# Optimization experiments

Hardware: AMD Instinct MI355X
Metric: run time of the kernel (lower is better)

Reference implementation:

```python
import jax, jax.numpy as jnp
import numpy as np

B, TS, TT = 32, 128, 64
V_SRC, V_TRG, E, H = 30000, 30000, 256, 512


def _cell(x, h, c, Wih, Whh, b):
    # x:[B,in], h,c:[B,H]; PyTorch gate order i,f,g,o
    g = x @ Wih.T + h @ Whh.T + b
    i, f, gg, o = jnp.split(g, 4, axis=-1)
    c = jax.nn.sigmoid(f) * c + jax.nn.sigmoid(i) * jnp.tanh(gg)
    h = jax.nn.sigmoid(o) * jnp.tanh(c)
    return h, c


def _lstm2(xs, p0, p1, state):
    # xs: [T,B,in]; 2-layer LSTM (dropout disabled / eval mode)
    def step(carry, x):
        h0, c0, h1, c1 = carry
        h0, c0 = _cell(x, h0, c0, *p0)
        h1, c1 = _cell(h0, h1, c1, *p1)
        return (h0, c0, h1, c1), h1
    carry, ys = jax.lax.scan(step, state, xs)
    return ys, carry


def setup_inputs() -> dict:
    key = jax.random.key(0)
    ks = jax.random.split(key, 28)
    n = lambda k, s: jax.random.normal(k, s, dtype=jnp.float32) * 0.05
    inp = {
        'src': jax.random.randint(ks[0], (B, TS), 0, V_SRC),
        'trg': jax.random.randint(ks[1], (B, TT), 0, V_TRG),
        'enc_emb': n(ks[2], (V_SRC, E)),
        'dec_emb': n(ks[3], (V_TRG, E)),
        'enc_Wih0': n(ks[4], (4 * H, E)), 'enc_Whh0': n(ks[5], (4 * H, H)),
        'enc_b0': n(ks[6], (4 * H,)),
        'enc_Wih1': n(ks[7], (4 * H, H)), 'enc_Whh1': n(ks[8], (4 * H, H)),
        'enc_b1': n(ks[9], (4 * H,)),
        'dec_Wih0': n(ks[10], (4 * H, E)), 'dec_Whh0': n(ks[11], (4 * H, H)),
        'dec_b0': n(ks[12], (4 * H,)),
        'dec_Wih1': n(ks[13], (4 * H, H)), 'dec_Whh1': n(ks[14], (4 * H, H)),
        'dec_b1': n(ks[15], (4 * H,)),
        'fc_W': n(ks[16], (V_TRG, H)), 'fc_b': n(ks[17], (V_TRG,)),
    }
    return inp


def reference(src, trg, enc_emb, dec_emb,
              enc_Wih0, enc_Whh0, enc_b0, enc_Wih1, enc_Whh1, enc_b1,
              dec_Wih0, dec_Whh0, dec_b0, dec_Wih1, dec_Whh1, dec_b1,
              fc_W, fc_b):
    zero = jnp.zeros((B, H), dtype=jnp.float32)
    # ---- Encoder ----
    src_e = enc_emb[src]                       # [B,TS,E]
    _, enc_state = _lstm2(jnp.swapaxes(src_e, 0, 1),
                          (enc_Wih0, enc_Whh0, enc_b0),
                          (enc_Wih1, enc_Whh1, enc_b1),
                          (zero, zero, zero, zero))
    # ---- Decoder (teacher forcing = 1.0): inputs trg[:, :-1] ----
    dec_in = dec_emb[trg[:, :-1]]              # [B,TT-1,E]
    hs, _ = _lstm2(jnp.swapaxes(dec_in, 0, 1),
                   (dec_Wih0, dec_Whh0, dec_b0),
                   (dec_Wih1, dec_Whh1, dec_b1),
                   enc_state)                  # hs: [TT-1,B,H]
    logits = jnp.einsum('tbh,vh->btv', hs, fc_W) + fc_b  # [B,TT-1,V]
    # outputs[:,0,:] stays zero as in original
    out = jnp.concatenate([jnp.zeros((B, 1, V_TRG), dtype=jnp.float32), logits], axis=1)
    return out
```

## Files before the change

### kernel.cpp

```cpp
#include <hip/hip_runtime.h>
#include <hip/hip_bf16.h>

#define B_SZ 32
#define TS 128
#define TT 64
#define TD 63
#define E_DIM 256
#define H_DIM 512
#define G4 2048
#define V_TRG 30000
#define NWG_L 32

typedef __attribute__((ext_vector_type(8))) short s8v;
typedef __attribute__((ext_vector_type(4))) float f32x4;
typedef unsigned short u16;
typedef unsigned long long u64;

static __device__ __forceinline__ float sigf(float x) {
  x = fminf(fmaxf(x, -30.f), 30.f);
  return 1.0f / (1.0f + __expf(-x));
}
static __device__ __forceinline__ float tanh_(float x) {
  x = fminf(fmaxf(x, -15.f), 15.f);
  float e = __expf(2.0f * x);
  return (e - 1.0f) / (e + 1.0f);
}
static __device__ __forceinline__ u16 f2bf(float x) {
  union { float f; unsigned u; } v; v.f = x;
  unsigned r = v.u + 0x7FFF + ((v.u >> 16) & 1);
  return (u16)(r >> 16);
}

struct Cvt { const float* s; u16* d; int n; };
struct Cvt9 { Cvt m[9]; };

__global__ void cvt_kernel(Cvt9 c) {
  const Cvt cv = c.m[blockIdx.y];
  int i = blockIdx.x * 256 + threadIdx.x;
  const int stride = gridDim.x * 256;
  for (; i < cv.n; i += stride) cv.d[i] = f2bf(cv.s[i]);
}

__global__ void embed_kernel(const int* __restrict__ tok, const float* __restrict__ emb,
                             u16* __restrict__ x, int rows, int tstride) {
  int i = blockIdx.x * 256 + threadIdx.x;
  if (i >= rows * E_DIM) return;
  int e = i & (E_DIM - 1);
  int r = i >> 8;
  int b = r & 31, t = r >> 5;
  int token = tok[b * tstride + t];
  x[i] = f2bf(emb[token * E_DIM + e]);
}

template<int MODE>
__global__ __launch_bounds__(256) void gemm_bf16(
    const u16* __restrict__ A, const u16* __restrict__ Bw,
    const float* __restrict__ bias, float* __restrict__ out,
    int M, int N, int K) {
  __shared__ u16 As[128 * 40];
  __shared__ u16 Bs[128 * 40];
  const int nb = blockIdx.x, mb = blockIdx.y;
  const int tid = threadIdx.x;
  const int w = tid >> 6, lane = tid & 63, quad = lane >> 4, cc = lane & 15;
  const int wm = w & 1, wn = w >> 1;
  f32x4 acc[4][4] = {};

  for (int k0 = 0; k0 < K; k0 += 32) {
    #pragma unroll
    for (int i = tid; i < 512; i += 256) {
      int m = i >> 2, kk = (i & 3) << 3;
      int gm = mb * 128 + m;
      s8v va = {};
      if (gm < M) va = *(const s8v*)(A + (size_t)gm * K + k0 + kk);
      *(s8v*)(&As[m * 40 + kk]) = va;
      int gn = nb * 128 + m;
      s8v vb = {};
      if (gn < N) vb = *(const s8v*)(Bw + (size_t)gn * K + k0 + kk);
      *(s8v*)(&Bs[m * 40 + kk]) = vb;
    }
    __syncthreads();
    s8v af[4], bf[4];
    #pragma unroll
    for (int mt = 0; mt < 4; ++mt)
      af[mt] = *(const s8v*)(&As[(wm * 64 + mt * 16 + cc) * 40 + quad * 8]);
    #pragma unroll
    for (int nt = 0; nt < 4; ++nt)
      bf[nt] = *(const s8v*)(&Bs[(wn * 64 + nt * 16 + cc) * 40 + quad * 8]);
    #pragma unroll
    for (int mt = 0; mt < 4; ++mt)
      #pragma unroll
      for (int nt = 0; nt < 4; ++nt)
        acc[mt][nt] = __builtin_amdgcn_mfma_f32_16x16x32_bf16(af[mt], bf[nt], acc[mt][nt], 0, 0, 0);
    __syncthreads();
  }

  #pragma unroll
  for (int mt = 0; mt < 4; ++mt)
    #pragma unroll
    for (int nt = 0; nt < 4; ++nt) {
      int col = nb * 128 + wn * 64 + nt * 16 + cc;
      if (col >= N) continue;
      float bv = bias[col];
      #pragma unroll
      for (int r = 0; r < 4; ++r) {
        int row = mb * 128 + wm * 64 + mt * 16 + quad * 4 + r;
        if (row >= M) continue;
        float v = acc[mt][nt][r] + bv;
        if (MODE == 0) {
          out[(size_t)row * N + col] = v;
        } else {
          int t = row >> 5, b = row & 31;
          out[(size_t)b * (TT * V_TRG) + (size_t)(t + 1) * V_TRG + col] = v;
        }
      }
    }
}

static __device__ __forceinline__ void spin_until(int* p, int target) {
  while (__hip_atomic_load(p, __ATOMIC_RELAXED, __HIP_MEMORY_SCOPE_AGENT) < target)
    __builtin_amdgcn_s_sleep(1);
}

__global__ __launch_bounds__(128, 1) void lstm2_scan(
    const float* __restrict__ Gx,
    const u16* __restrict__ Whh0,
    const u16* __restrict__ Wih1,
    const u16* __restrict__ Whh1,
    const float* __restrict__ b1,
    const u16* __restrict__ h0i, const float* __restrict__ c0i,
    const u16* __restrict__ h1i, const float* __restrict__ c1i,
    u16* __restrict__ H0x,
    u16* __restrict__ H1x,
    u16* __restrict__ h0f, float* __restrict__ c0f,
    u16* __restrict__ h1f, float* __restrict__ c1f,
    int T, int* bar0, int* bar1) {
  __shared__ u16 BsH[64 * 512];
  __shared__ u16 BsX[64 * 512];
  const bool L1 = (blockIdx.x >= NWG_L);
  const int jn = blockIdx.x & 31;
  const int tid = threadIdx.x;
  const int mt = tid >> 6, lane = tid & 63, quad = lane >> 4, cc = lane & 15;

  {
    const u16* Wh = L1 ? Whh1 : Whh0;
    for (int i = tid; i < 64 * 64; i += 128) {
      int col = i >> 6, kc = i & 63;
      int g = col >> 4, c = col & 15;
      int row = g * 512 + jn * 16 + c;
      s8v v = *(const s8v*)(Wh + (size_t)row * 512 + kc * 8);
      int kcs = (kc + col) & 63;
      *(s8v*)(&BsH[col * 512 + kcs * 8]) = v;
    }
    if (L1) {
      for (int i = tid; i < 64 * 64; i += 128) {
        int col = i >> 6, kc = i & 63;
        int g = col >> 4, c = col & 15;
        int row = g * 512 + jn * 16 + c;
        s8v v = *(const s8v*)(Wih1 + (size_t)row * 512 + kc * 8);
        int kcs = (kc + col) & 63;
        *(s8v*)(&BsX[col * 512 + kcs * 8]) = v;
      }
    }
  }
  __syncthreads();

  const int b0 = mt * 16 + quad * 4;
  const int j = jn * 16 + cc;
  const int arow = (mt * 16 + cc) * H_DIM + quad * 8;

  f32x4 creg;
  {
    const float* ci = L1 ? c1i : c0i;
    #pragma unroll
    for (int r = 0; r < 4; ++r) creg[r] = ci[(b0 + r) * H_DIM + j];
  }

  if (!L1) {
    for (int s = 0; s < T; ++s) {
      float gx[4][4];
      #pragma unroll
      for (int g = 0; g < 4; ++g)
        #pragma unroll
        for (int r = 0; r < 4; ++r)
          gx[g][r] = Gx[(size_t)(s * B_SZ + b0 + r) * G4 + g * 512 + j];

      if (s > 0) {
        spin_until(bar0, NWG_L * s);
        asm volatile("" ::: "memory");
      }
      const u16* hsrc = (s == 0) ? h0i : (H0x + (size_t)(s - 1) * (B_SZ * H_DIM));
      f32x4 acc[4] = {};
      #pragma unroll
      for (int ks = 0; ks < 16; ++ks) {
        s8v a = *(const s8v*)(hsrc + arow + ks * 32);
        int kc = ks * 4 + quad;
        #pragma unroll
        for (int g = 0; g < 4; ++g) {
          int col = g * 16 + cc;
          int kcs = (kc + col) & 63;
          s8v bw = *(const s8v*)(&BsH[col * 512 + kcs * 8]);
          acc[g] = __builtin_amdgcn_mfma_f32_16x16x32_bf16(a, bw, acc[g], 0, 0, 0);
        }
      }
      u16* hw = H0x + (size_t)s * (B_SZ * H_DIM);
      #pragma unroll
      for (int r = 0; r < 4; ++r) {
        float gi = acc[0][r] + gx[0][r];
        float gf = acc[1][r] + gx[1][r];
        float gg = acc[2][r] + gx[2][r];
        float go = acc[3][r] + gx[3][r];
        float cn = sigf(gf) * creg[r] + sigf(gi) * tanh_(gg);
        float hn = sigf(go) * tanh_(cn);
        creg[r] = cn;
        u16 hb = f2bf(hn);
        __hip_atomic_store(&hw[(b0 + r) * H_DIM + j], hb,
                           __ATOMIC_RELAXED, __HIP_MEMORY_SCOPE_AGENT);
        if (s == T - 1) {
          h0f[(b0 + r) * H_DIM + j] = hb;
          c0f[(b0 + r) * H_DIM + j] = cn;
        }
      }
      __syncthreads();
      if (tid == 0)
        __hip_atomic_fetch_add(bar0, 1, __ATOMIC_RELAXED, __HIP_MEMORY_SCOPE_AGENT);
    }
  } else {
    float bv4[4];
    #pragma unroll
    for (int g = 0; g < 4; ++g) bv4[g] = b1[g * 512 + j];

    for (int s = 0; s < T; ++s) {
      spin_until(bar0, NWG_L * (s + 1));
      asm volatile("" ::: "memory");
      const u16* h0src = H0x + (size_t)s * (B_SZ * H_DIM);
      s8v a0r[16];
      #pragma unroll
      for (int ks = 0; ks < 16; ++ks)
        a0r[ks] = *(const s8v*)(h0src + arow + ks * 32);

      if (s > 0) {
        spin_until(bar1, NWG_L * s);
        asm volatile("" ::: "memory");
      }
      const u16* h1src = (s == 0) ? h1i : (H1x + (size_t)(s - 1) * (B_SZ * H_DIM));
      f32x4 acc[4] = {};
      #pragma unroll
      for (int ks = 0; ks < 16; ++ks) {
        s8v a1 = *(const s8v*)(h1src + arow + ks * 32);
        int kc = ks * 4 + quad;
        #pragma unroll
        for (int g = 0; g < 4; ++g) {
          int col = g * 16 + cc;
          int kcs = (kc + col) & 63;
          s8v bh = *(const s8v*)(&BsH[col * 512 + kcs * 8]);
          s8v bx = *(const s8v*)(&BsX[col * 512 + kcs * 8]);
          acc[g] = __builtin_amdgcn_mfma_f32_16x16x32_bf16(a1, bh, acc[g], 0, 0, 0);
          acc[g] = __builtin_amdgcn_mfma_f32_16x16x32_bf16(a0r[ks], bx, acc[g], 0, 0, 0);
        }
      }
      u16* hw = H1x + (size_t)s * (B_SZ * H_DIM);
      #pragma unroll
      for (int r = 0; r < 4; ++r) {
        float gi = acc[0][r] + bv4[0];
        float gf = acc[1][r] + bv4[1];
        float gg = acc[2][r] + bv4[2];
        float go = acc[3][r] + bv4[3];
        float cn = sigf(gf) * creg[r] + sigf(gi) * tanh_(gg);
        float hn = sigf(go) * tanh_(cn);
        creg[r] = cn;
        u16 hb = f2bf(hn);
        __hip_atomic_store(&hw[(b0 + r) * H_DIM + j], hb,
                           __ATOMIC_RELAXED, __HIP_MEMORY_SCOPE_AGENT);
        if (s == T - 1) {
          h1f[(b0 + r) * H_DIM + j] = hb;
          c1f[(b0 + r) * H_DIM + j] = cn;
        }
      }
      __syncthreads();
      if (tid == 0 && s < T - 1)
        __hip_atomic_fetch_add(bar1, 1, __ATOMIC_RELAXED, __HIP_MEMORY_SCOPE_AGENT);
    }
  }
}

__global__ void zero_t0_kernel(float* __restrict__ out) {
  int i = blockIdx.x * 256 + threadIdx.x;
  if (i >= B_SZ * V_TRG) return;
  int b = i / V_TRG, v = i - b * V_TRG;
  out[(size_t)b * (TT * V_TRG) + v] = 0.f;
}

extern "C" void kernel_launch(void* const* d_in, const int* in_sizes, int n_in,
                              void* d_out, int out_size, void* d_ws, size_t ws_size,
                              hipStream_t stream) {
  const int*   src     = (const int*)d_in[0];
  const int*   trg     = (const int*)d_in[1];
  const float* enc_emb = (const float*)d_in[2];
  const float* dec_emb = (const float*)d_in[3];
  const float* eW0i = (const float*)d_in[4];
  const float* eW0h = (const float*)d_in[5];
  const float* eb0  = (const float*)d_in[6];
  const float* eW1i = (const float*)d_in[7];
  const float* eW1h = (const float*)d_in[8];
  const float* eb1  = (const float*)d_in[9];
  const float* dW0i = (const float*)d_in[10];
  const float* dW0h = (const float*)d_in[11];
  const float* db0  = (const float*)d_in[12];
  const float* dW1i = (const float*)d_in[13];
  const float* dW1h = (const float*)d_in[14];
  const float* db1  = (const float*)d_in[15];
  const float* fcW  = (const float*)d_in[16];
  const float* fcb  = (const float*)d_in[17];
  float* out = (float*)d_out;

  char* ws = (char*)d_ws;
  size_t off = 0;
  auto alloc = [&](size_t bytes) {
    char* p = ws + off;
    off = (off + bytes + 255) & ~(size_t)255;
    return p;
  };
  int*   bar    = (int*)alloc(1024);
  u16*   hzero  = (u16*)alloc(B_SZ * H_DIM * 2);
  float* czero  = (float*)alloc(B_SZ * H_DIM * 4);
  u16* eW0i_b = (u16*)alloc((size_t)G4 * E_DIM * 2);
  u16* eW0h_b = (u16*)alloc((size_t)G4 * H_DIM * 2);
  u16* eW1i_b = (u16*)alloc((size_t)G4 * H_DIM * 2);
  u16* eW1h_b = (u16*)alloc((size_t)G4 * H_DIM * 2);
  u16* dW0i_b = (u16*)alloc((size_t)G4 * E_DIM * 2);
  u16* dW0h_b = (u16*)alloc((size_t)G4 * H_DIM * 2);
  u16* dW1i_b = (u16*)alloc((size_t)G4 * H_DIM * 2);
  u16* dW1h_b = (u16*)alloc((size_t)G4 * H_DIM * 2);
  u16* fcW_b  = (u16*)alloc((size_t)V_TRG * H_DIM * 2);
  u16* x_enc  = (u16*)alloc((size_t)TS * B_SZ * E_DIM * 2);
  u16* x_dec  = (u16*)alloc((size_t)TD * B_SZ * E_DIM * 2);
  float* Gx   = (float*)alloc((size_t)TS * B_SZ * G4 * 4);
  u16* H0e    = (u16*)alloc((size_t)TS * B_SZ * H_DIM * 2);
  u16* H1e    = (u16*)alloc((size_t)TS * B_SZ * H_DIM * 2);
  u16* H0d    = (u16*)alloc((size_t)TD * B_SZ * H_DIM * 2);
  u16* H1d    = (u16*)alloc((size_t)TD * B_SZ * H_DIM * 2);
  u16* hF0    = (u16*)alloc(B_SZ * H_DIM * 2);
  float* cF0  = (float*)alloc(B_SZ * H_DIM * 4);
  u16* hF1    = (u16*)alloc(B_SZ * H_DIM * 2);
  float* cF1  = (float*)alloc(B_SZ * H_DIM * 4);
  u16* hFd0   = (u16*)alloc(B_SZ * H_DIM * 2);
  float* cFd0 = (float*)alloc(B_SZ * H_DIM * 4);
  u16* hFd1   = (u16*)alloc(B_SZ * H_DIM * 2);
  float* cFd1 = (float*)alloc(B_SZ * H_DIM * 4);

  hipMemsetAsync(bar, 0, 1024, stream);
  hipMemsetAsync(hzero, 0, B_SZ * H_DIM * 2, stream);
  hipMemsetAsync(czero, 0, B_SZ * H_DIM * 4, stream);

  Cvt9 c9 = {{ {eW0i, eW0i_b, G4 * E_DIM}, {eW0h, eW0h_b, G4 * H_DIM},
               {eW1i, eW1i_b, G4 * H_DIM}, {eW1h, eW1h_b, G4 * H_DIM},
               {dW0i, dW0i_b, G4 * E_DIM}, {dW0h, dW0h_b, G4 * H_DIM},
               {dW1i, dW1i_b, G4 * H_DIM}, {dW1h, dW1h_b, G4 * H_DIM},
               {fcW,  fcW_b,  V_TRG * H_DIM} }};
  cvt_kernel<<<dim3(1024, 9), 256, 0, stream>>>(c9);

  embed_kernel<<<(TS * B_SZ * E_DIM + 255) / 256, 256, 0, stream>>>(src, enc_emb, x_enc, TS * B_SZ, TS);
  embed_kernel<<<(TD * B_SZ * E_DIM + 255) / 256, 256, 0, stream>>>(trg, dec_emb, x_dec, TD * B_SZ, TT);

  gemm_bf16<0><<<dim3(16, 32), 256, 0, stream>>>(x_enc, eW0i_b, eb0, Gx, TS * B_SZ, G4, E_DIM);
  lstm2_scan<<<2 * NWG_L, 128, 0, stream>>>(
      Gx, eW0h_b, eW1i_b, eW1h_b, eb1,
      hzero, czero, hzero, czero,
      H0e, H1e, hF0, cF0, hF1, cF1, TS, bar + 0, bar + 32);

  gemm_bf16<0><<<dim3(16, 16), 256, 0, stream>>>(x_dec, dW0i_b, db0, Gx, TD * B_SZ, G4, E_DIM);
  lstm2_scan<<<2 * NWG_L, 128, 0, stream>>>(
      Gx, dW0h_b, dW1i_b, dW1h_b, db1,
      hF0, cF0, hF1, cF1,
      H0d, H1d, hFd0, cFd0, hFd1, cFd1, TD, bar + 64, bar + 96);

  gemm_bf16<1><<<dim3((V_TRG + 127) / 128, (TD * B_SZ + 127) / 128), 256, 0, stream>>>(
      H1d, fcW_b, fcb, out, TD * B_SZ, V_TRG, H_DIM);
  zero_t0_kernel<<<(B_SZ * V_TRG + 255) / 256, 256, 0, stream>>>(out);
}
```

Measured before the change: 1.808 ms.

## Replace counter barriers with per-element tagged hidden states and fuse input projection

Hidden states are now stored as 32-bit words that pack the bf16 value with a timestep tag. Consumers poll the data directly until every tag matches, which removes the atomic counter barriers and the __syncthreads before each signal. The layer-0 input projection (the x·Wih0 GEMM) now runs inside the scan kernel using Wih0 held in shared memory, so the separate Gx GEMM launches and the large Gx buffer go away. In exchange, the state buffers double in size and need a memset, per-step polling loads become wider, and the decoder writes an extra plain bf16 copy of h1 for the output projection.

```diff
diff --git a/kernel.cpp b/kernel.cpp
--- a/kernel.cpp
+++ b/kernel.cpp
@@ -14,6 +14,7 @@
 typedef __attribute__((ext_vector_type(8))) short s8v;
 typedef __attribute__((ext_vector_type(4))) float f32x4;
 typedef unsigned short u16;
+typedef unsigned int u32;
 typedef unsigned long long u64;
 
 static __device__ __forceinline__ float sigf(float x) {
@@ -116,24 +117,44 @@
     }
 }
 
-static __device__ __forceinline__ void spin_until(int* p, int target) {
-  while (__hip_atomic_load(p, __ATOMIC_RELAXED, __HIP_MEMORY_SCOPE_AGENT) < target)
-    __builtin_amdgcn_s_sleep(1);
+union PK { u32 w[4]; s8v v; };
+
+static __device__ __forceinline__ void poll16(const u32* __restrict__ base, u32 tag, PK* a) {
+  const u64 tp  = (u64)tag | ((u64)tag << 32);
+  const u64 MSK = 0x0000FFFF0000FFFFULL;
+  for (;;) {
+    u64 bad = 0;
+    #pragma unroll
+    for (int ks = 0; ks < 16; ++ks) {
+      const u64* p = (const u64*)(base + ks * 32);
+      #pragma unroll
+      for (int i = 0; i < 4; ++i) {
+        u64 q = __hip_atomic_load(p + i, __ATOMIC_RELAXED, __HIP_MEMORY_SCOPE_AGENT);
+        bad |= (q ^ tp) & MSK;
+        a[ks].w[i] = (u32)(((q >> 16) & 0xFFFFULL) | ((q >> 32) & 0xFFFF0000ULL));
+      }
+    }
+    if (!__any(bad != 0)) return;
+    __builtin_amdgcn_s_sleep(2);
+  }
 }
 
 __global__ __launch_bounds__(128, 1) void lstm2_scan(
-    const float* __restrict__ Gx,
+    const u16* __restrict__ X,
+    const u16* __restrict__ Wih0,
     const u16* __restrict__ Whh0,
+    const float* __restrict__ bias0,
     const u16* __restrict__ Wih1,
     const u16* __restrict__ Whh1,
-    const float* __restrict__ b1,
+    const float* __restrict__ bias1,
     const u16* __restrict__ h0i, const float* __restrict__ c0i,
     const u16* __restrict__ h1i, const float* __restrict__ c1i,
-    u16* __restrict__ H0x,
-    u16* __restrict__ H1x,
+    u32* __restrict__ H0x,
+    u32* __restrict__ H1x,
+    u16* __restrict__ Hplain,
     u16* __restrict__ h0f, float* __restrict__ c0f,
     u16* __restrict__ h1f, float* __restrict__ c1f,
-    int T, int* bar0, int* bar1) {
+    int T) {
   __shared__ u16 BsH[64 * 512];
   __shared__ u16 BsX[64 * 512];
   const bool L1 = (blockIdx.x >= NWG_L);
@@ -145,120 +166,80 @@
     const u16* Wh = L1 ? Whh1 : Whh0;
     for (int i = tid; i < 64 * 64; i += 128) {
       int col = i >> 6, kc = i & 63;
-      int g = col >> 4, c = col & 15;
-      int row = g * 512 + jn * 16 + c;
+      int row = (col >> 4) * 512 + jn * 16 + (col & 15);
       s8v v = *(const s8v*)(Wh + (size_t)row * 512 + kc * 8);
-      int kcs = (kc + col) & 63;
-      *(s8v*)(&BsH[col * 512 + kcs * 8]) = v;
+      *(s8v*)(&BsH[col * 512 + ((kc + col) & 63) * 8]) = v;
     }
     if (L1) {
       for (int i = tid; i < 64 * 64; i += 128) {
         int col = i >> 6, kc = i & 63;
-        int g = col >> 4, c = col & 15;
-        int row = g * 512 + jn * 16 + c;
+        int row = (col >> 4) * 512 + jn * 16 + (col & 15);
         s8v v = *(const s8v*)(Wih1 + (size_t)row * 512 + kc * 8);
-        int kcs = (kc + col) & 63;
-        *(s8v*)(&BsX[col * 512 + kcs * 8]) = v;
+        *(s8v*)(&BsX[col * 512 + ((kc + col) & 63) * 8]) = v;
+      }
+    } else {
+      for (int i = tid; i < 64 * 32; i += 128) {
+        int col = i >> 5, kc = i & 31;
+        int row = (col >> 4) * 512 + jn * 16 + (col & 15);
+        s8v v = *(const s8v*)(Wih0 + (size_t)row * 256 + kc * 8);
+        *(s8v*)(&BsX[col * 256 + ((kc + col) & 31) * 8]) = v;
       }
     }
   }
   __syncthreads();
 
-  const int b0 = mt * 16 + quad * 4;
-  const int j = jn * 16 + cc;
+  const int br = mt * 16 + quad * 4;
+  const int j  = jn * 16 + cc;
   const int arow = (mt * 16 + cc) * H_DIM + quad * 8;
+
+  const float* biasp = L1 ? bias1 : bias0;
+  float bv4[4];
+  #pragma unroll
+  for (int g = 0; g < 4; ++g) bv4[g] = biasp[g * 512 + j];
 
   f32x4 creg;
   {
     const float* ci = L1 ? c1i : c0i;
     #pragma unroll
-    for (int r = 0; r < 4; ++r) creg[r] = ci[(b0 + r) * H_DIM + j];
+    for (int r = 0; r < 4; ++r) creg[r] = ci[(br + r) * H_DIM + j];
   }
+
+  PK a[16];
 
   if (!L1) {
     for (int s = 0; s < T; ++s) {
-      float gx[4][4];
-      #pragma unroll
-      for (int g = 0; g < 4; ++g)
-        #pragma unroll
-        for (int r = 0; r < 4; ++r)
-          gx[g][r] = Gx[(size_t)(s * B_SZ + b0 + r) * G4 + g * 512 + j];
-
-      if (s > 0) {
-        spin_until(bar0, NWG_L * s);
-        asm volatile("" ::: "memory");
-      }
-      const u16* hsrc = (s == 0) ? h0i : (H0x + (size_t)(s - 1) * (B_SZ * H_DIM));
       f32x4 acc[4] = {};
-      #pragma unroll
-      for (int ks = 0; ks < 16; ++ks) {
-        s8v a = *(const s8v*)(hsrc + arow + ks * 32);
+      const u16* xrow = X + ((size_t)(s * B_SZ) + mt * 16 + cc) * E_DIM + quad * 8;
+      #pragma unroll
+      for (int ks = 0; ks < 8; ++ks) {
+        s8v xa = *(const s8v*)(xrow + ks * 32);
         int kc = ks * 4 + quad;
         #pragma unroll
         for (int g = 0; g < 4; ++g) {
           int col = g * 16 + cc;
-          int kcs = (kc + col) & 63;
-          s8v bw = *(const s8v*)(&BsH[col * 512 + kcs * 8]);
-          acc[g] = __builtin_amdgcn_mfma_f32_16x16x32_bf16(a, bw, acc[g], 0, 0, 0);
-        }
-      }
-      u16* hw = H0x + (size_t)s * (B_SZ * H_DIM);
-      #pragma unroll
-      for (int r = 0; r < 4; ++r) {
-        float gi = acc[0][r] + gx[0][r];
-        float gf = acc[1][r] + gx[1][r];
-        float gg = acc[2][r] + gx[2][r];
-        float go = acc[3][r] + gx[3][r];
-        float cn = sigf(gf) * creg[r] + sigf(gi) * tanh_(gg);
-        float hn = sigf(go) * tanh_(cn);
-        creg[r] = cn;
-        u16 hb = f2bf(hn);
-        __hip_atomic_store(&hw[(b0 + r) * H_DIM + j], hb,
-                           __ATOMIC_RELAXED, __HIP_MEMORY_SCOPE_AGENT);
-        if (s == T - 1) {
-          h0f[(b0 + r) * H_DIM + j] = hb;
-          c0f[(b0 + r) * H_DIM + j] = cn;
-        }
-      }
-      __syncthreads();
-      if (tid == 0)
-        __hip_atomic_fetch_add(bar0, 1, __ATOMIC_RELAXED, __HIP_MEMORY_SCOPE_AGENT);
-    }
-  } else {
-    float bv4[4];
-    #pragma unroll
-    for (int g = 0; g < 4; ++g) bv4[g] = b1[g * 512 + j];
-
-    for (int s = 0; s < T; ++s) {
-      spin_until(bar0, NWG_L * (s + 1));
-      asm volatile("" ::: "memory");
-      const u16* h0src = H0x + (size_t)s * (B_SZ * H_DIM);
-      s8v a0r[16];
-      #pragma unroll
-      for (int ks = 0; ks < 16; ++ks)
-        a0r[ks] = *(const s8v*)(h0src + arow + ks * 32);
-
-      if (s > 0) {
-        spin_until(bar1, NWG_L * s);
-        asm volatile("" ::: "memory");
-      }
-      const u16* h1src = (s == 0) ? h1i : (H1x + (size_t)(s - 1) * (B_SZ * H_DIM));
-      f32x4 acc[4] = {};
+          s8v bx = *(const s8v*)(&BsX[col * 256 + ((kc + col) & 31) * 8]);
+          acc[g] = __builtin_amdgcn_mfma_f32_16x16x32_bf16(xa, bx, acc[g], 0, 0, 0);
+        }
+      }
+      if (s == 0) {
+        #pragma unroll
+        for (int ks = 0; ks < 16; ++ks)
+          a[ks].v = *(const s8v*)(h0i + arow + ks * 32);
+      } else {
+        poll16(H0x + (size_t)(s - 1) * (B_SZ * H_DIM) + arow, (u32)s, a);
+      }
       #pragma unroll
       for (int ks = 0; ks < 16; ++ks) {
-        s8v a1 = *(const s8v*)(h1src + arow + ks * 32);
         int kc = ks * 4 + quad;
         #pragma unroll
         for (int g = 0; g < 4; ++g) {
           int col = g * 16 + cc;
-          int kcs = (kc + col) & 63;
-          s8v bh = *(const s8v*)(&BsH[col * 512 + kcs * 8]);
-          s8v bx = *(const s8v*)(&BsX[col * 512 + kcs * 8]);
-          acc[g] = __builtin_amdgcn_mfma_f32_16x16x32_bf16(a1, bh, acc[g], 0, 0, 0);
-          acc[g] = __builtin_amdgcn_mfma_f32_16x16x32_bf16(a0r[ks], bx, acc[g], 0, 0, 0);
-        }
-      }
-      u16* hw = H1x + (size_t)s * (B_SZ * H_DIM);
+          s8v bh = *(const s8v*)(&BsH[col * 512 + ((kc + col) & 63) * 8]);
+          acc[g] = __builtin_amdgcn_mfma_f32_16x16x32_bf16(a[ks].v, bh, acc[g], 0, 0, 0);
+        }
+      }
+      u32* hw = H0x + (size_t)s * (B_SZ * H_DIM);
+      const u32 tg = (u32)(s + 1);
       #pragma unroll
       for (int r = 0; r < 4; ++r) {
         float gi = acc[0][r] + bv4[0];
@@ -269,16 +250,66 @@
         float hn = sigf(go) * tanh_(cn);
         creg[r] = cn;
         u16 hb = f2bf(hn);
-        __hip_atomic_store(&hw[(b0 + r) * H_DIM + j], hb,
+        __hip_atomic_store(&hw[(br + r) * H_DIM + j], ((u32)hb << 16) | tg,
                            __ATOMIC_RELAXED, __HIP_MEMORY_SCOPE_AGENT);
-        if (s == T - 1) {
-          h1f[(b0 + r) * H_DIM + j] = hb;
-          c1f[(b0 + r) * H_DIM + j] = cn;
-        }
-      }
-      __syncthreads();
-      if (tid == 0 && s < T - 1)
-        __hip_atomic_fetch_add(bar1, 1, __ATOMIC_RELAXED, __HIP_MEMORY_SCOPE_AGENT);
+        if (s == T - 1 && h0f) {
+          h0f[(br + r) * H_DIM + j] = hb;
+          c0f[(br + r) * H_DIM + j] = cn;
+        }
+      }
+    }
+  } else {
+    for (int s = 0; s < T; ++s) {
+      f32x4 acc[4] = {};
+      poll16(H0x + (size_t)s * (B_SZ * H_DIM) + arow, (u32)(s + 1), a);
+      #pragma unroll
+      for (int ks = 0; ks < 16; ++ks) {
+        int kc = ks * 4 + quad;
+        #pragma unroll
+        for (int g = 0; g < 4; ++g) {
+          int col = g * 16 + cc;
+          s8v bx = *(const s8v*)(&BsX[col * 512 + ((kc + col) & 63) * 8]);
+          acc[g] = __builtin_amdgcn_mfma_f32_16x16x32_bf16(a[ks].v, bx, acc[g], 0, 0, 0);
+        }
+      }
+      if (s == 0) {
+        #pragma unroll
+        for (int ks = 0; ks < 16; ++ks)
+          a[ks].v = *(const s8v*)(h1i + arow + ks * 32);
+      } else {
+        poll16(H1x + (size_t)(s - 1) * (B_SZ * H_DIM) + arow, (u32)s, a);
+      }
+      #pragma unroll
+      for (int ks = 0; ks < 16; ++ks) {
+        int kc = ks * 4 + quad;
+        #pragma unroll
+        for (int g = 0; g < 4; ++g) {
+          int col = g * 16 + cc;
+          s8v bh = *(const s8v*)(&BsH[col * 512 + ((kc + col) & 63) * 8]);
+          acc[g] = __builtin_amdgcn_mfma_f32_16x16x32_bf16(a[ks].v, bh, acc[g], 0, 0, 0);
+        }
+      }
+      u32* hw = H1x + (size_t)s * (B_SZ * H_DIM);
+      const u32 tg = (u32)(s + 1);
+      #pragma unroll
+      for (int r = 0; r < 4; ++r) {
+        float gi = acc[0][r] + bv4[0];
+        float gf = acc[1][r] + bv4[1];
+        float gg = acc[2][r] + bv4[2];
+        float go = acc[3][r] + bv4[3];
+        float cn = sigf(gf) * creg[r] + sigf(gi) * tanh_(gg);
+        float hn = sigf(go) * tanh_(cn);
+        creg[r] = cn;
+        u16 hb = f2bf(hn);
+        __hip_atomic_store(&hw[(br + r) * H_DIM + j], ((u32)hb << 16) | tg,
+                           __ATOMIC_RELAXED, __HIP_MEMORY_SCOPE_AGENT);
+        if (Hplain)
+          Hplain[(size_t)(s * B_SZ + br + r) * H_DIM + j] = hb;
+        if (s == T - 1 && h1f) {
+          h1f[(br + r) * H_DIM + j] = hb;
+          c1f[(br + r) * H_DIM + j] = cn;
+        }
+      }
     }
   }
 }
@@ -320,7 +351,6 @@
     off = (off + bytes + 255) & ~(size_t)255;
     return p;
   };
-  int*   bar    = (int*)alloc(1024);
   u16*   hzero  = (u16*)alloc(B_SZ * H_DIM * 2);
   float* czero  = (float*)alloc(B_SZ * H_DIM * 4);
   u16* eW0i_b = (u16*)alloc((size_t)G4 * E_DIM * 2);
@@ -334,23 +364,22 @@
   u16* fcW_b  = (u16*)alloc((size_t)V_TRG * H_DIM * 2);
   u16* x_enc  = (u16*)alloc((size_t)TS * B_SZ * E_DIM * 2);
   u16* x_dec  = (u16*)alloc((size_t)TD * B_SZ * E_DIM * 2);
-  float* Gx   = (float*)alloc((size_t)TS * B_SZ * G4 * 4);
-  u16* H0e    = (u16*)alloc((size_t)TS * B_SZ * H_DIM * 2);
-  u16* H1e    = (u16*)alloc((size_t)TS * B_SZ * H_DIM * 2);
-  u16* H0d    = (u16*)alloc((size_t)TD * B_SZ * H_DIM * 2);
-  u16* H1d    = (u16*)alloc((size_t)TD * B_SZ * H_DIM * 2);
+  const size_t PLANE_E = (size_t)TS * B_SZ * H_DIM;
+  const size_t PLANE_D = (size_t)TD * B_SZ * H_DIM;
+  u32* tagbase = (u32*)alloc((2 * PLANE_E + 2 * PLANE_D) * 4);
+  u32* H0e = tagbase;
+  u32* H1e = H0e + PLANE_E;
+  u32* H0d = H1e + PLANE_E;
+  u32* H1d = H0d + PLANE_D;
+  u16* H1d_p  = (u16*)alloc((size_t)TD * B_SZ * H_DIM * 2);
   u16* hF0    = (u16*)alloc(B_SZ * H_DIM * 2);
   float* cF0  = (float*)alloc(B_SZ * H_DIM * 4);
   u16* hF1    = (u16*)alloc(B_SZ * H_DIM * 2);
   float* cF1  = (float*)alloc(B_SZ * H_DIM * 4);
-  u16* hFd0   = (u16*)alloc(B_SZ * H_DIM * 2);
-  float* cFd0 = (float*)alloc(B_SZ * H_DIM * 4);
-  u16* hFd1   = (u16*)alloc(B_SZ * H_DIM * 2);
-  float* cFd1 = (float*)alloc(B_SZ * H_DIM * 4);
-
-  hipMemsetAsync(bar, 0, 1024, stream);
+
   hipMemsetAsync(hzero, 0, B_SZ * H_DIM * 2, stream);
   hipMemsetAsync(czero, 0, B_SZ * H_DIM * 4, stream);
+  hipMemsetAsync(tagbase, 0, (2 * PLANE_E + 2 * PLANE_D) * 4, stream);
 
   Cvt9 c9 = {{ {eW0i, eW0i_b, G4 * E_DIM}, {eW0h, eW0h_b, G4 * H_DIM},
                {eW1i, eW1i_b, G4 * H_DIM}, {eW1h, eW1h_b, G4 * H_DIM},
@@ -362,19 +391,19 @@
   embed_kernel<<<(TS * B_SZ * E_DIM + 255) / 256, 256, 0, stream>>>(src, enc_emb, x_enc, TS * B_SZ, TS);
   embed_kernel<<<(TD * B_SZ * E_DIM + 255) / 256, 256, 0, stream>>>(trg, dec_emb, x_dec, TD * B_SZ, TT);
 
-  gemm_bf16<0><<<dim3(16, 32), 256, 0, stream>>>(x_enc, eW0i_b, eb0, Gx, TS * B_SZ, G4, E_DIM);
   lstm2_scan<<<2 * NWG_L, 128, 0, stream>>>(
-      Gx, eW0h_b, eW1i_b, eW1h_b, eb1,
+      x_enc, eW0i_b, eW0h_b, eb0, eW1i_b, eW1h_b, eb1,
       hzero, czero, hzero, czero,
-      H0e, H1e, hF0, cF0, hF1, cF1, TS, bar + 0, bar + 32);
-
-  gemm_bf16<0><<<dim3(16, 16), 256, 0, stream>>>(x_dec, dW0i_b, db0, Gx, TD * B_SZ, G4, E_DIM);
+      H0e, H1e, (u16*)nullptr,
+      hF0, cF0, hF1, cF1, TS);
+
   lstm2_scan<<<2 * NWG_L, 128, 0, stream>>>(
-      Gx, dW0h_b, dW1i_b, dW1h_b, db1,
+      x_dec, dW0i_b, dW0h_b, db0, dW1i_b, dW1h_b, db1,
       hF0, cF0, hF1, cF1,
-      H0d, H1d, hFd0, cFd0, hFd1, cFd1, TD, bar + 64, bar + 96);
+      H0d, H1d, H1d_p,
+      (u16*)nullptr, (float*)nullptr, (u16*)nullptr, (float*)nullptr, TD);
 
   gemm_bf16<1><<<dim3((V_TRG + 127) / 128, (TD * B_SZ + 127) / 128), 256, 0, stream>>>(
-      H1d, fcW_b, fcb, out, TD * B_SZ, V_TRG, H_DIM);
+      H1d_p, fcW_b, fcb, out, TD * B_SZ, V_TRG, H_DIM);
   zero_t0_kernel<<<(B_SZ * V_TRG + 255) / 256, 256, 0, stream>>>(out);
 }
```

Measured after the change: 2.185 ms. 1.21x slower.
